# Optimization experiments

Measured on AMD Instinct MI355X. Metric: run time of the kernel, lower is better.

Reference implementation:

```python
import jax, jax.numpy as jnp
import numpy as np

EPS = 1e-6


def setup_inputs() -> dict:
    key = jax.random.key(0)
    k_x, k_qkv, k_proj = jax.random.split(key, 3)
    B, C, H, W, D = 4, 256, 16, 16, 16
    x = jax.random.normal(k_x, (B, C, H, W, D), dtype=jnp.float32)
    # 1x1 Conv3d == per-position linear; init roughly like torch conv default
    fan_in = C
    bound = 1.0 / np.sqrt(fan_in)
    qkv_w = jax.random.uniform(k_qkv, (3 * C, C), jnp.float32, -bound, bound)
    qkv_b = jnp.zeros((3 * C,), jnp.float32)
    proj_w = jax.random.uniform(k_proj, (C, C), jnp.float32, -bound, bound)
    proj_b = jnp.zeros((C,), jnp.float32)
    norm_gamma = jnp.ones((C,), jnp.float32)
    norm_beta = jnp.zeros((C,), jnp.float32)
    return {"x": x, "norm_gamma": norm_gamma, "norm_beta": norm_beta,
            "qkv_w": qkv_w, "qkv_b": qkv_b, "proj_w": proj_w, "proj_b": proj_b}


def reference(x, norm_gamma, norm_beta, qkv_w, qkv_b, proj_w, proj_b):
    B, C, H, W, D = x.shape
    N = H * W * D
    scale = float(C) ** -0.5

    # GroupNorm with num_groups=1: normalize over (C,H,W,D) per sample (biased var)
    mean = jnp.mean(x, axis=(1, 2, 3, 4), keepdims=True)
    var = jnp.mean(jnp.square(x - mean), axis=(1, 2, 3, 4), keepdims=True)
    xn = (x - mean) * jax.lax.rsqrt(var + EPS)
    xn = xn * norm_gamma[None, :, None, None, None] + norm_beta[None, :, None, None, None]

    xn_flat = xn.reshape(B, C, N)  # b c n
    # 1x1 conv == channel-mixing GEMM
    qkv = jnp.einsum('oc,bcn->bon', qkv_w, xn_flat) + qkv_b[None, :, None]  # [B, 3C, N]
    q, k, v = jnp.split(qkv, 3, axis=1)  # each [B, C, N]

    w = jnp.einsum('bcq,bck->bqk', q, k) * scale  # [B, N, N]
    w = jax.nn.softmax(w, axis=-1)
    h = jnp.einsum('bqk,bck->bcq', w, v)  # [B, C, N]

    h = jnp.einsum('oc,bcn->bon', proj_w, h) + proj_b[None, :, None]
    return x + h.reshape(B, C, H, W, D)
```

## Files before the change

### kernel.cpp

```cpp
#include <hip/hip_runtime.h>

typedef __attribute__((ext_vector_type(8))) short short8;
typedef __attribute__((ext_vector_type(4))) float f32x4;
typedef __attribute__((ext_vector_type(16))) float f32x16;
typedef __attribute__((ext_vector_type(4))) int i32x4;

__device__ __forceinline__ unsigned short f2bf(float f){
  union { float f; unsigned int u; } cv; cv.f = f;
  unsigned int u = cv.u;
  u = (u + 0x7fffu + ((u >> 16) & 1u)) >> 16;
  return (unsigned short)u;
}
__device__ __forceinline__ float bf2f(unsigned short h){
  union { unsigned int u; float f; } cv; cv.u = ((unsigned int)h) << 16;
  return cv.f;
}

typedef unsigned int u32g __attribute__((address_space(1)));
typedef unsigned int u32l __attribute__((address_space(3)));
__device__ __forceinline__ void gload16(const void* g, void* l){
  __builtin_amdgcn_global_load_lds((const u32g*)g, (u32l*)l, 16, 0, 0);
}

__device__ __forceinline__ unsigned int cvt2_fp8(float a, float b){
  unsigned int r;
  asm("v_cvt_pk_fp8_f32 %0, %1, %2" : "=v"(r) : "v"(a), "v"(b));
  return r;
}

#define BARRIER() asm volatile("s_barrier" ::: "memory")
#define WAITV(N)  asm volatile("s_waitcnt vmcnt(" #N ")" ::: "memory")

__global__ __launch_bounds__(256) void fused_pre_k(const float* __restrict__ x,
                                                   float2* __restrict__ partial,
                                                   const float* __restrict__ qkv_w,
                                                   const float* __restrict__ qkv_b,
                                                   const float* __restrict__ proj_w,
                                                   unsigned short* __restrict__ Wqk,
                                                   unsigned short* __restrict__ Wv,
                                                   unsigned short* __restrict__ Wp,
                                                   float* __restrict__ bias_qkv){
  const int blk = blockIdx.x;
  if (blk < 256){
    const int b = blk >> 6, xb = blk & 63;
    const float4* xp = (const float4*)(x + (size_t)b*1048576 + (size_t)xb*16384);
    float s = 0.f, sq = 0.f;
    #pragma unroll
    for (int i = 0; i < 16; ++i){
      float4 v = xp[threadIdx.x + i*256];
      s  += v.x + v.y + v.z + v.w;
      sq += v.x*v.x + v.y*v.y + v.z*v.z + v.w*v.w;
    }
    #pragma unroll
    for (int m = 1; m < 64; m <<= 1){ s += __shfl_xor(s, m); sq += __shfl_xor(sq, m); }
    __shared__ float2 acc[4];
    if ((threadIdx.x & 63) == 0) acc[threadIdx.x >> 6] = make_float2(s, sq);
    __syncthreads();
    if (threadIdx.x == 0){
      float S = 0.f, Q = 0.f;
      for (int i = 0; i < 4; ++i){ S += acc[i].x; Q += acc[i].y; }
      partial[b*64 + xb] = make_float2(S, Q);
    }
  } else {
    int id = (blk - 256) * 256 + threadIdx.x;
    if (id < 131072){
      Wqk[id] = f2bf(qkv_w[id]);
      if (id < 768) bias_qkv[id] = qkv_b[id];
    } else if (id < 196608){
      Wv[id - 131072] = f2bf(qkv_w[id]);
    } else {
      int j = id - 196608;
      Wp[j] = f2bf(proj_w[j]);
    }
  }
}

__global__ __launch_bounds__(256) void norm_transpose_k(const float* __restrict__ x,
                                                        const float* __restrict__ gamma,
                                                        const float* __restrict__ beta,
                                                        const float2* __restrict__ partial,
                                                        unsigned short* __restrict__ xnt){
  __shared__ float tile[64][65];
  __shared__ float2 stt;
  const int b = blockIdx.z, n0 = blockIdx.x*64, c0 = blockIdx.y*64;
  const int t = threadIdx.x;
  if (t < 64){
    float2 p = partial[b*64 + t];
    float s = p.x, q = p.y;
    #pragma unroll
    for (int m = 1; m < 64; m <<= 1){ s += __shfl_xor(s, m); q += __shfl_xor(q, m); }
    if (t == 0){
      const float inv = 1.0f/1048576.0f;
      float mean = s*inv;
      float var  = q*inv - mean*mean;
      stt = make_float2(mean, rsqrtf(var + 1e-6f));
    }
  }
  __syncthreads();
  const float2 st = stt;
  const int col = t & 63, rb = t >> 6;
  #pragma unroll
  for (int i = 0; i < 16; ++i){
    int rr = i*4 + rb;
    float xv = x[((size_t)b*256 + c0 + rr)*4096 + n0 + col];
    tile[rr][col] = (xv - st.x) * st.y * gamma[c0+rr] + beta[c0+rr];
  }
  __syncthreads();
  #pragma unroll
  for (int i = 0; i < 16; ++i){
    int nr = i*4 + rb;
    xnt[((size_t)b*4096 + n0 + nr)*256 + c0 + col] = f2bf(tile[col][nr]);
  }
}

__global__ __launch_bounds__(256) void gemm_nt_k(const unsigned short* __restrict__ A,
                                                 const unsigned short* __restrict__ B,
                                                 int lda, int ldb, long sA, long sB,
                                                 const float* __restrict__ bias_m,
                                                 const float* __restrict__ bias_n,
                                                 const float* __restrict__ resid, long sR,
                                                 float* __restrict__ outF,
                                                 unsigned short* __restrict__ outB,
                                                 unsigned char* __restrict__ out8,
                                                 unsigned char* __restrict__ out8v,
                                                 int ldc, long sC, int vtile){
  __shared__ unsigned short As[64][40];
  __shared__ unsigned short Bs[64][40];
  const int b  = blockIdx.z;
  const int m0 = blockIdx.x * 64, n0 = blockIdx.y * 64;
  const unsigned short* Ab = A + (size_t)b * sA;
  const unsigned short* Bb = B + (size_t)b * sB;
  const int t = threadIdx.x;
  const int lane = t & 63, w = t >> 6;
  const int g = lane >> 4, r = lane & 15;
  const int wm = (w >> 1) * 32, wn = (w & 1) * 32;
  const int lrow = t >> 2, lcol = (t & 3) * 8;
  f32x4 acc00 = {0,0,0,0}, acc01 = {0,0,0,0}, acc10 = {0,0,0,0}, acc11 = {0,0,0,0};
  for (int ks = 0; ks < 8; ++ks){
    short8 av = *(const short8*)(Ab + (size_t)(m0 + lrow) * lda + ks*32 + lcol);
    short8 bv = *(const short8*)(Bb + (size_t)(n0 + lrow) * ldb + ks*32 + lcol);
    __syncthreads();
    *(short8*)&As[lrow][lcol] = av;
    *(short8*)&Bs[lrow][lcol] = bv;
    __syncthreads();
    short8 af0 = *(const short8*)&As[wm + r][g*8];
    short8 af1 = *(const short8*)&As[wm + 16 + r][g*8];
    short8 bf0 = *(const short8*)&Bs[wn + r][g*8];
    short8 bf1 = *(const short8*)&Bs[wn + 16 + r][g*8];
    acc00 = __builtin_amdgcn_mfma_f32_16x16x32_bf16(af0, bf0, acc00, 0, 0, 0);
    acc01 = __builtin_amdgcn_mfma_f32_16x16x32_bf16(af0, bf1, acc01, 0, 0, 0);
    acc10 = __builtin_amdgcn_mfma_f32_16x16x32_bf16(af1, bf0, acc10, 0, 0, 0);
    acc11 = __builtin_amdgcn_mfma_f32_16x16x32_bf16(af1, bf1, acc11, 0, 0, 0);
  }
  f32x4 accs[2][2] = {{acc00, acc01},{acc10, acc11}};
  #pragma unroll
  for (int mi = 0; mi < 2; ++mi)
    #pragma unroll
    for (int ni = 0; ni < 2; ++ni)
      #pragma unroll
      for (int j = 0; j < 4; ++j){
        int gm = m0 + wm + mi*16 + g*4 + j;
        int gn = n0 + wn + ni*16 + r;
        float vv = accs[mi][ni][j];
        if (bias_m) vv += bias_m[gm];
        if (bias_n) vv += bias_n[gn];
        if (resid)  vv += resid[(size_t)b*sR + (size_t)gm*ldc + gn];
        if (out8){
          unsigned char v8 = (unsigned char)(cvt2_fp8(vv, vv) & 0xff);
          if (vtile == 3 && gn >= 512){
            int c = gn - 512, n = gm;
            int inner = (((c & 31)*16 + (n & 15)) ^ (((c >> 3) & 1) << 3));
            out8v[(size_t)b*1048576 + (size_t)((n >> 4)*8 + (c >> 5))*512 + inner] = v8;
          } else {
            out8[(size_t)b*sC + (size_t)gm*ldc + gn] = v8;
          }
        } else if (outB){
          outB[(size_t)b*sC + (size_t)gm*ldc + gn] = f2bf(vv);
        } else {
          outF[(size_t)b*sC + (size_t)gm*ldc + gn] = vv;
        }
      }
}

__global__ __launch_bounds__(256, 2) void attn_k(const unsigned char* __restrict__ qk8,
                                                 const unsigned char* __restrict__ vt8,
                                                 unsigned short* __restrict__ po,
                                                 float* __restrict__ ml){
  __shared__ __align__(16) char smem[32768];
  const int id = blockIdx.x;
  const int combo = id & 15, qb = id >> 4;
  const int b = combo >> 2, ks = combo & 3;
  const int q0 = qb * 128;
  const int t = threadIdx.x, lane = t & 63, w = t >> 6;
  const int hi = lane >> 5, l31 = lane & 31;
  const unsigned char* qkb = qk8 + (size_t)b * 4096 * 512;
  const unsigned char* vtb = vt8 + (size_t)b * 1048576;
  const float SQL2 = 0.0625f * 1.44269504088896340736f;

  unsigned long long qf[16];
  {
    const unsigned char* qrow = qkb + (size_t)(q0 + w*32 + l31) * 512;
    #pragma unroll
    for (int s = 0; s < 16; ++s) qf[s] = *(const unsigned long long*)(qrow + s*16 + hi*8);
  }

  auto stageK = [&](int kt, char* buf){
    const int kbase = ks*1024 + kt*32;
    #pragma unroll
    for (int i2 = 0; i2 < 2; ++i2){
      int ci = (w*2 + i2)*64 + lane;
      int r = ci >> 4;
      const unsigned char* src = qkb + (size_t)(kbase + r)*512 + 256
                               + (((ci & 15) ^ (r & 15)) * 16);
      gload16(src, buf + (w*2 + i2)*1024);
    }
  };
  auto stageV = [&](int kt, char* buf){
    const int kbase = ks*1024 + kt*32;
    #pragma unroll
    for (int i = 0; i < 2; ++i){
      int tp = (w*2 + i)*2;
      int tile = tp + (lane >> 5);
      const unsigned char* src = vtb + (size_t)((kbase >> 4) + (tile >> 3))*4096
                               + (tile & 7)*512 + (lane & 31)*16;
      gload16(src, buf + 8192 + tp*512);
    }
  };
  stageK(0, smem);
  stageV(0, smem);

  f32x16 O[8];
  #pragma unroll
  for (int cb = 0; cb < 8; ++cb)
    #pragma unroll
    for (int jj = 0; jj < 16; ++jj) O[cb][jj] = 0.f;
  float lrun = 0.f;
  const int ksw = (l31 & 15) << 4;
  const int vsw = ((l31 >> 3) & 1) << 3;
  const int vbase = l31*16 + hi*8;

  for (int kt = 0; kt < 32; ++kt){
    char* cur = smem + (kt & 1)*16384;
    char* nxt = smem + ((kt + 1) & 1)*16384;

    WAITV(0);
    BARRIER();

    int ktn = (kt < 31) ? kt + 1 : 31;
    stageK(ktn, nxt);
    stageV(ktn, nxt);

    f32x16 Sa, Sb;
    #pragma unroll
    for (int jj = 0; jj < 16; ++jj){ Sa[jj] = 0.f; Sb[jj] = 0.f; }
    const char* kp = cur + l31*256;
    __builtin_amdgcn_s_setprio(1);
    #pragma unroll
    for (int s = 0; s < 8; ++s){
      unsigned long long k0 = *(const unsigned long long*)(kp + (((2*s  )*16 + hi*8) ^ ksw));
      unsigned long long k1 = *(const unsigned long long*)(kp + (((2*s+1)*16 + hi*8) ^ ksw));
      Sa = __builtin_amdgcn_mfma_f32_32x32x16_fp8_fp8((long long)k0, (long long)qf[2*s  ], Sa, 0, 0, 0);
      Sb = __builtin_amdgcn_mfma_f32_32x32x16_fp8_fp8((long long)k1, (long long)qf[2*s+1], Sb, 0, 0, 0);
    }
    __builtin_amdgcn_s_setprio(0);

    float p[16];
    #pragma unroll
    for (int jj = 0; jj < 16; ++jj)
      p[jj] = __builtin_amdgcn_exp2f((Sa[jj] + Sb[jj]) * SQL2);
    lrun += ((p[0]+p[1]) + (p[2]+p[3])) + ((p[4]+p[5]) + (p[6]+p[7]))
          + ((p[8]+p[9]) + (p[10]+p[11])) + ((p[12]+p[13]) + (p[14]+p[15]));
    unsigned A0 = (unsigned)__builtin_amdgcn_cvt_pk_fp8_f32(p[0],  p[1],  0, false);
    A0 = (unsigned)__builtin_amdgcn_cvt_pk_fp8_f32(p[2],  p[3],  (int)A0, true);
    unsigned B0 = (unsigned)__builtin_amdgcn_cvt_pk_fp8_f32(p[4],  p[5],  0, false);
    B0 = (unsigned)__builtin_amdgcn_cvt_pk_fp8_f32(p[6],  p[7],  (int)B0, true);
    unsigned A1 = (unsigned)__builtin_amdgcn_cvt_pk_fp8_f32(p[8],  p[9],  0, false);
    A1 = (unsigned)__builtin_amdgcn_cvt_pk_fp8_f32(p[10], p[11], (int)A1, true);
    unsigned B1 = (unsigned)__builtin_amdgcn_cvt_pk_fp8_f32(p[12], p[13], 0, false);
    B1 = (unsigned)__builtin_amdgcn_cvt_pk_fp8_f32(p[14], p[15], (int)B1, true);
    asm("v_permlane32_swap_b32 %0, %1" : "+v"(A0), "+v"(B0));
    asm("v_permlane32_swap_b32 %0, %1" : "+v"(A1), "+v"(B1));
    long long pb0 = (long long)(((unsigned long long)B0 << 32) | A0);
    long long pb1 = (long long)(((unsigned long long)B1 << 32) | A1);

    const char* Vt = cur + 8192;
    __builtin_amdgcn_s_setprio(1);
    #pragma unroll
    for (int cb = 0; cb < 8; ++cb){
      unsigned long long v0 = *(const unsigned long long*)(Vt + (0*8 + cb)*512 + (vbase ^ vsw));
      O[cb] = __builtin_amdgcn_mfma_f32_32x32x16_fp8_fp8((long long)v0, pb0, O[cb], 0, 0, 0);
      unsigned long long v1 = *(const unsigned long long*)(Vt + (1*8 + cb)*512 + (vbase ^ vsw));
      O[cb] = __builtin_amdgcn_mfma_f32_32x32x16_fp8_fp8((long long)v1, pb1, O[cb], 0, 0, 0);
    }
    __builtin_amdgcn_s_setprio(0);
  }
  WAITV(0);

  float lf = lrun + __shfl_xor(lrun, 32);
  const int qg = q0 + w*32 + l31;
  unsigned short* pob = po + (size_t)combo * 1048576;
  #pragma unroll
  for (int cb = 0; cb < 8; ++cb)
    #pragma unroll
    for (int jj = 0; jj < 16; ++jj){
      int c = cb*32 + (jj & 3) + 8*(jj >> 2) + 4*hi;
      pob[(size_t)c*4096 + qg] = f2bf(O[cb][jj]);
    }
  if (lane < 32)
    ml[(size_t)combo*4096 + qg] = lf;
}

__global__ __launch_bounds__(256) void attn_merge_k(const unsigned short* __restrict__ po,
                                                    const float* __restrict__ ml,
                                                    unsigned short* __restrict__ ho){
  __shared__ float Of[64][261];
  const int b = blockIdx.y, q0 = blockIdx.x * 64;
  const int t = threadIdx.x, ql = t & 63, ci = t >> 6;
  const int q = q0 + ql;
  float L = 0.f;
  #pragma unroll
  for (int ksv = 0; ksv < 4; ++ksv)
    L += ml[(size_t)(b*4 + ksv)*4096 + q];
  float inv = 1.0f / L;
  float acc[64];
  #pragma unroll
  for (int i = 0; i < 64; ++i) acc[i] = 0.f;
  #pragma unroll
  for (int ksv = 0; ksv < 4; ++ksv){
    const unsigned short* pb = po + (size_t)(b*4 + ksv)*1048576 + q;
    #pragma unroll
    for (int i = 0; i < 64; ++i)
      acc[i] += bf2f(pb[(size_t)(ci + 4*i)*4096]);
  }
  #pragma unroll
  for (int i = 0; i < 64; ++i) Of[ql][ci + 4*i] = acc[i] * inv;
  __syncthreads();
  const int qr = t >> 2, sub = t & 3;
  const float* rowp = Of[qr];
  unsigned short* dst = ho + ((size_t)(b*4096 + q0 + qr))*256;
  #pragma unroll
  for (int jj = 0; jj < 8; ++jj){
    int c = sub*8 + jj*32;
    float4 v0 = *(const float4*)(rowp + c);
    float4 v1 = *(const float4*)(rowp + c + 4);
    short8 o;
    o[0] = (short)f2bf(v0.x); o[1] = (short)f2bf(v0.y);
    o[2] = (short)f2bf(v0.z); o[3] = (short)f2bf(v0.w);
    o[4] = (short)f2bf(v1.x); o[5] = (short)f2bf(v1.y);
    o[6] = (short)f2bf(v1.z); o[7] = (short)f2bf(v1.w);
    *(short8*)(dst + c) = o;
  }
}

extern "C" void kernel_launch(void* const* d_in, const int* in_sizes, int n_in,
                              void* d_out, int out_size, void* d_ws, size_t ws_size,
                              hipStream_t stream){
  const float* x      = (const float*)d_in[0];
  const float* gamma  = (const float*)d_in[1];
  const float* beta   = (const float*)d_in[2];
  const float* qkv_w  = (const float*)d_in[3];
  const float* qkv_b  = (const float*)d_in[4];
  const float* proj_w = (const float*)d_in[5];
  const float* proj_b = (const float*)d_in[6];
  float* out = (float*)d_out;
  char* ws = (char*)d_ws;

  float2* partial        = (float2*)(ws + 0);
  float*  bias_qkv       = (float*)(ws + 4096);
  unsigned short* Wqk    = (unsigned short*)(ws + 8192);
  unsigned short* Wv     = (unsigned short*)(ws + 270336);
  unsigned short* Wp     = (unsigned short*)(ws + 401408);
  unsigned short* xnt    = (unsigned short*)(ws + 532480);
  unsigned char*  qk8    = (unsigned char*)(ws + 8921088);
  unsigned char*  vt8    = (unsigned char*)(ws + 17309696);
  unsigned short* po     = (unsigned short*)(ws + 25698304);
  float*          ml     = (float*)(ws + 59252736);
  unsigned short* ho     = xnt;

  fused_pre_k<<<1280, 256, 0, stream>>>(x, partial, qkv_w, qkv_b, proj_w,
                                        Wqk, Wv, Wp, bias_qkv);
  norm_transpose_k<<<dim3(64,4,4), 256, 0, stream>>>(x, gamma, beta, partial, xnt);
  gemm_nt_k<<<dim3(64,12,4), 256, 0, stream>>>(xnt, Wqk, 256, 256, 4096L*256, 0,
      nullptr, bias_qkv, nullptr, 0, nullptr, nullptr, qk8, vt8, 512, 4096L*512, 3);
  attn_k<<<dim3(512), 256, 0, stream>>>(qk8, vt8, po, ml);
  attn_merge_k<<<dim3(64,4), 256, 0, stream>>>(po, ml, ho);
  gemm_nt_k<<<dim3(4,64,4), 256, 0, stream>>>(Wp, ho, 256, 256, 0, 4096L*256,
      proj_b, nullptr, x, 1048576L, out, nullptr, nullptr, nullptr, 4096, 1048576L, 0);
}
```

Baseline: 124.5 us.

## Double-buffer gemm_nt tiles via direct global-to-LDS loads with XOR swizzle

Replaces the register-staged load/store into padded LDS arrays with global_load_lds direct transfers into a double-buffered shared region. The next K-slice is prefetched while the current one is consumed, and a single barrier per iteration replaces two. An XOR swizzle on the 16-byte column chunks avoids bank conflicts without padding. The cost is twice the LDS footprint and a reliance on WAITV/BARRIER macros being correct for the async loads.

```diff
diff --git a/kernel.cpp b/kernel.cpp
--- a/kernel.cpp
+++ b/kernel.cpp
@@ -124,8 +124,7 @@
                                                  unsigned char* __restrict__ out8,
                                                  unsigned char* __restrict__ out8v,
                                                  int ldc, long sC, int vtile){
-  __shared__ unsigned short As[64][40];
-  __shared__ unsigned short Bs[64][40];
+  __shared__ __align__(16) char gs[16384];
   const int b  = blockIdx.z;
   const int m0 = blockIdx.x * 64, n0 = blockIdx.y * 64;
   const unsigned short* Ab = A + (size_t)b * sA;
@@ -134,19 +133,37 @@
   const int lane = t & 63, w = t >> 6;
   const int g = lane >> 4, r = lane & 15;
   const int wm = (w >> 1) * 32, wn = (w & 1) * 32;
-  const int lrow = t >> 2, lcol = (t & 3) * 8;
+  const int srow = lane >> 2;
+  const int scol = ((lane & 3) ^ (srow & 3)) * 8;
+  auto stage = [&](int ks, int half){
+    char* buf = gs + half*8192;
+    if (w < 2){
+      #pragma unroll
+      for (int i = 0; i < 2; ++i){
+        int m = w*32 + i*16 + srow;
+        gload16(Ab + (size_t)(m0 + m)*lda + ks*32 + scol, buf + w*2048 + i*1024);
+      }
+    } else {
+      #pragma unroll
+      for (int i = 0; i < 2; ++i){
+        int n = (w-2)*32 + i*16 + srow;
+        gload16(Bb + (size_t)(n0 + n)*ldb + ks*32 + scol, buf + 4096 + (w-2)*2048 + i*1024);
+      }
+    }
+  };
+  stage(0, 0);
   f32x4 acc00 = {0,0,0,0}, acc01 = {0,0,0,0}, acc10 = {0,0,0,0}, acc11 = {0,0,0,0};
+  const int sa = (g ^ (r & 3)) << 4;
   for (int ks = 0; ks < 8; ++ks){
-    short8 av = *(const short8*)(Ab + (size_t)(m0 + lrow) * lda + ks*32 + lcol);
-    short8 bv = *(const short8*)(Bb + (size_t)(n0 + lrow) * ldb + ks*32 + lcol);
-    __syncthreads();
-    *(short8*)&As[lrow][lcol] = av;
-    *(short8*)&Bs[lrow][lcol] = bv;
-    __syncthreads();
-    short8 af0 = *(const short8*)&As[wm + r][g*8];
-    short8 af1 = *(const short8*)&As[wm + 16 + r][g*8];
-    short8 bf0 = *(const short8*)&Bs[wn + r][g*8];
-    short8 bf1 = *(const short8*)&Bs[wn + 16 + r][g*8];
+    WAITV(0);
+    BARRIER();
+    if (ks < 7) stage(ks + 1, (ks + 1) & 1);
+    const char* Abuf = gs + (ks & 1)*8192;
+    const char* Bbuf = Abuf + 4096;
+    short8 af0 = *(const short8*)(Abuf + (wm + r)*64 + sa);
+    short8 af1 = *(const short8*)(Abuf + (wm + 16 + r)*64 + sa);
+    short8 bf0 = *(const short8*)(Bbuf + (wn + r)*64 + sa);
+    short8 bf1 = *(const short8*)(Bbuf + (wn + 16 + r)*64 + sa);
     acc00 = __builtin_amdgcn_mfma_f32_16x16x32_bf16(af0, bf0, acc00, 0, 0, 0);
     acc01 = __builtin_amdgcn_mfma_f32_16x16x32_bf16(af0, bf1, acc01, 0, 0, 0);
     acc10 = __builtin_amdgcn_mfma_f32_16x16x32_bf16(af1, bf0, acc10, 0, 0, 0);
```

Result: no change. 126.1 us (+1.3%).

## Fuse split-K attention merge into output projection GEMM with packed bf16 partials

Applied to the files above, without the earlier changes.

Replaces the separate attention-merge kernel and the projection GEMM with one kernel that sums the four split-K partial outputs on the fly, feeds them as MFMA operands against double-buffered Wp tiles, and applies 1/L normalisation, bias and residual in the epilogue. The attention kernel now writes its partial outputs as packed 4×bf16 64-bit stores in a channel-group-major layout, using the hardware pack-convert instruction, instead of scalar 16-bit stores. The QKV GEMM is specialised to its single fp8 output path, dropping runtime branches. This removes one launch and the round trip of the merged bf16 tensor through memory. In exchange the merge work is tied to GEMM tiling, and the fused kernel re-reads partials with only 32 columns per block.

```diff
diff --git a/kernel.cpp b/kernel.cpp
--- a/kernel.cpp
+++ b/kernel.cpp
@@ -22,6 +22,11 @@
   __builtin_amdgcn_global_load_lds((const u32g*)g, (u32l*)l, 16, 0, 0);
 }
 
+__device__ __forceinline__ unsigned int cvtpk_bf16(float lo, float hi){
+  unsigned int r;
+  asm("v_cvt_pk_bf16_f32 %0, %1, %2" : "=v"(r) : "v"(lo), "v"(hi));
+  return r;
+}
 __device__ __forceinline__ unsigned int cvt2_fp8(float a, float b){
   unsigned int r;
   asm("v_cvt_pk_fp8_f32 %0, %1, %2" : "=v"(r) : "v"(a), "v"(b));
@@ -116,14 +121,10 @@
 __global__ __launch_bounds__(256) void gemm_nt_k(const unsigned short* __restrict__ A,
                                                  const unsigned short* __restrict__ B,
                                                  int lda, int ldb, long sA, long sB,
-                                                 const float* __restrict__ bias_m,
                                                  const float* __restrict__ bias_n,
-                                                 const float* __restrict__ resid, long sR,
-                                                 float* __restrict__ outF,
-                                                 unsigned short* __restrict__ outB,
                                                  unsigned char* __restrict__ out8,
                                                  unsigned char* __restrict__ out8v,
-                                                 int ldc, long sC, int vtile){
+                                                 int ldc, long sC){
   __shared__ unsigned short As[64][40];
   __shared__ unsigned short Bs[64][40];
   const int b  = blockIdx.z;
@@ -161,30 +162,21 @@
       for (int j = 0; j < 4; ++j){
         int gm = m0 + wm + mi*16 + g*4 + j;
         int gn = n0 + wn + ni*16 + r;
-        float vv = accs[mi][ni][j];
-        if (bias_m) vv += bias_m[gm];
-        if (bias_n) vv += bias_n[gn];
-        if (resid)  vv += resid[(size_t)b*sR + (size_t)gm*ldc + gn];
-        if (out8){
-          unsigned char v8 = (unsigned char)(cvt2_fp8(vv, vv) & 0xff);
-          if (vtile == 3 && gn >= 512){
-            int c = gn - 512, n = gm;
-            int inner = (((c & 31)*16 + (n & 15)) ^ (((c >> 3) & 1) << 3));
-            out8v[(size_t)b*1048576 + (size_t)((n >> 4)*8 + (c >> 5))*512 + inner] = v8;
-          } else {
-            out8[(size_t)b*sC + (size_t)gm*ldc + gn] = v8;
-          }
-        } else if (outB){
-          outB[(size_t)b*sC + (size_t)gm*ldc + gn] = f2bf(vv);
+        float vv = accs[mi][ni][j] + bias_n[gn];
+        unsigned char v8 = (unsigned char)(cvt2_fp8(vv, vv) & 0xff);
+        if (gn >= 512){
+          int c = gn - 512, n = gm;
+          int inner = (((c & 31)*16 + (n & 15)) ^ (((c >> 3) & 1) << 3));
+          out8v[(size_t)b*1048576 + (size_t)((n >> 4)*8 + (c >> 5))*512 + inner] = v8;
         } else {
-          outF[(size_t)b*sC + (size_t)gm*ldc + gn] = vv;
+          out8[(size_t)b*sC + (size_t)gm*ldc + gn] = v8;
         }
       }
 }
 
 __global__ __launch_bounds__(256, 2) void attn_k(const unsigned char* __restrict__ qk8,
                                                  const unsigned char* __restrict__ vt8,
-                                                 unsigned short* __restrict__ po,
+                                                 char* __restrict__ po4,
                                                  float* __restrict__ ml){
   __shared__ __align__(16) char smem[32768];
   const int id = blockIdx.x;
@@ -298,57 +290,102 @@
 
   float lf = lrun + __shfl_xor(lrun, 32);
   const int qg = q0 + w*32 + l31;
-  unsigned short* pob = po + (size_t)combo * 1048576;
+  unsigned long long* pob = (unsigned long long*)(po4 + (size_t)combo * 2097152);
   #pragma unroll
   for (int cb = 0; cb < 8; ++cb)
     #pragma unroll
-    for (int jj = 0; jj < 16; ++jj){
-      int c = cb*32 + (jj & 3) + 8*(jj >> 2) + 4*hi;
-      pob[(size_t)c*4096 + qg] = f2bf(O[cb][jj]);
+    for (int J = 0; J < 4; ++J){
+      unsigned lo = cvtpk_bf16(O[cb][4*J+0], O[cb][4*J+1]);
+      unsigned hi2 = cvtpk_bf16(O[cb][4*J+2], O[cb][4*J+3]);
+      int cg = cb*8 + J*2 + hi;
+      pob[(size_t)cg*4096 + qg] = ((unsigned long long)hi2 << 32) | lo;
     }
   if (lane < 32)
     ml[(size_t)combo*4096 + qg] = lf;
 }
 
-__global__ __launch_bounds__(256) void attn_merge_k(const unsigned short* __restrict__ po,
-                                                    const float* __restrict__ ml,
-                                                    unsigned short* __restrict__ ho){
-  __shared__ float Of[64][261];
-  const int b = blockIdx.y, q0 = blockIdx.x * 64;
-  const int t = threadIdx.x, ql = t & 63, ci = t >> 6;
-  const int q = q0 + ql;
+__global__ __launch_bounds__(256, 2) void projm_k(const char* __restrict__ po4,
+                                                  const float* __restrict__ ml,
+                                                  const unsigned short* __restrict__ Wp,
+                                                  const float* __restrict__ proj_b,
+                                                  const float* __restrict__ x,
+                                                  float* __restrict__ out){
+  __shared__ __align__(16) char wsm[32768];
+  const int b = blockIdx.y, n0 = blockIdx.x * 32;
+  const int t = threadIdx.x, lane = t & 63, w = t >> 6;
+  const int hi = lane >> 5, l31 = lane & 31;
+  const int n = n0 + l31;
+
   float L = 0.f;
   #pragma unroll
-  for (int ksv = 0; ksv < 4; ++ksv)
-    L += ml[(size_t)(b*4 + ksv)*4096 + q];
+  for (int ksv = 0; ksv < 4; ++ksv) L += ml[(size_t)(b*4 + ksv)*4096 + n];
   float inv = 1.0f / L;
-  float acc[64];
-  #pragma unroll
-  for (int i = 0; i < 64; ++i) acc[i] = 0.f;
-  #pragma unroll
-  for (int ksv = 0; ksv < 4; ++ksv){
-    const unsigned short* pb = po + (size_t)(b*4 + ksv)*1048576 + q;
-    #pragma unroll
-    for (int i = 0; i < 64; ++i)
-      acc[i] += bf2f(pb[(size_t)(ci + 4*i)*4096]);
-  }
-  #pragma unroll
-  for (int i = 0; i < 64; ++i) Of[ql][ci + 4*i] = acc[i] * inv;
-  __syncthreads();
-  const int qr = t >> 2, sub = t & 3;
-  const float* rowp = Of[qr];
-  unsigned short* dst = ho + ((size_t)(b*4096 + q0 + qr))*256;
-  #pragma unroll
-  for (int jj = 0; jj < 8; ++jj){
-    int c = sub*8 + jj*32;
-    float4 v0 = *(const float4*)(rowp + c);
-    float4 v1 = *(const float4*)(rowp + c + 4);
-    short8 o;
-    o[0] = (short)f2bf(v0.x); o[1] = (short)f2bf(v0.y);
-    o[2] = (short)f2bf(v0.z); o[3] = (short)f2bf(v0.w);
-    o[4] = (short)f2bf(v1.x); o[5] = (short)f2bf(v1.y);
-    o[6] = (short)f2bf(v1.z); o[7] = (short)f2bf(v1.w);
-    *(short8*)(dst + c) = o;
+
+  const char* pob[4];
+  #pragma unroll
+  for (int ksv = 0; ksv < 4; ++ksv) pob[ksv] = po4 + (size_t)(b*4 + ksv)*2097152;
+
+  auto stageW = [&](int kstep, char* buf){
+    #pragma unroll
+    for (int i = 0; i < 4; ++i){
+      int tile = w*4 + i, ot = tile >> 1, ks2 = tile & 1;
+      const unsigned short* src = Wp + (size_t)(ot*32 + l31)*256 + kstep*32 + ks2*16 + hi*8;
+      gload16(src, buf + tile*1024);
+    }
+  };
+  stageW(0, wsm);
+
+  f32x16 acc0, acc1;
+  #pragma unroll
+  for (int jj = 0; jj < 16; ++jj){ acc0[jj] = 0.f; acc1[jj] = 0.f; }
+
+  for (int kstep = 0; kstep < 8; ++kstep){
+    char* cur = wsm + (kstep & 1)*16384;
+    char* nxt = wsm + ((kstep + 1) & 1)*16384;
+    WAITV(0);
+    BARRIER();
+    if (kstep < 7) stageW(kstep + 1, nxt);
+
+    short8 hf[2];
+    #pragma unroll
+    for (int ks2 = 0; ks2 < 2; ++ks2){
+      int cg = kstep*8 + ks2*4 + hi*2;
+      float s[8];
+      #pragma unroll
+      for (int j = 0; j < 8; ++j) s[j] = 0.f;
+      #pragma unroll
+      for (int ksv = 0; ksv < 4; ++ksv){
+        unsigned long long a = *(const unsigned long long*)(pob[ksv] + ((size_t)cg*4096 + n)*8);
+        unsigned long long c = *(const unsigned long long*)(pob[ksv] + ((size_t)(cg+1)*4096 + n)*8);
+        s[0] += bf2f((unsigned short)a);        s[1] += bf2f((unsigned short)(a >> 16));
+        s[2] += bf2f((unsigned short)(a >> 32));s[3] += bf2f((unsigned short)(a >> 48));
+        s[4] += bf2f((unsigned short)c);        s[5] += bf2f((unsigned short)(c >> 16));
+        s[6] += bf2f((unsigned short)(c >> 32));s[7] += bf2f((unsigned short)(c >> 48));
+      }
+      unsigned u0 = cvtpk_bf16(s[0], s[1]), u1 = cvtpk_bf16(s[2], s[3]);
+      unsigned u2 = cvtpk_bf16(s[4], s[5]), u3 = cvtpk_bf16(s[6], s[7]);
+      i32x4 uv = {(int)u0, (int)u1, (int)u2, (int)u3};
+      hf[ks2] = __builtin_bit_cast(short8, uv);
+    }
+
+    #pragma unroll
+    for (int ks2 = 0; ks2 < 2; ++ks2){
+      short8 wf0 = *(const short8*)(cur + ((w*2 + 0)*2 + ks2)*1024 + lane*16);
+      acc0 = __builtin_amdgcn_mfma_f32_32x32x16_bf16(wf0, hf[ks2], acc0, 0, 0, 0);
+      short8 wf1 = *(const short8*)(cur + ((w*2 + 1)*2 + ks2)*1024 + lane*16);
+      acc1 = __builtin_amdgcn_mfma_f32_32x32x16_bf16(wf1, hf[ks2], acc1, 0, 0, 0);
+    }
+  }
+
+  #pragma unroll
+  for (int ot = 0; ot < 2; ++ot){
+    const f32x16& A = ot ? acc1 : acc0;
+    #pragma unroll
+    for (int jj = 0; jj < 16; ++jj){
+      int o = w*64 + ot*32 + (jj & 3) + 8*(jj >> 2) + 4*hi;
+      size_t off = ((size_t)(b*256 + o))*4096 + n;
+      out[off] = A[jj]*inv + proj_b[o] + x[off];
+    }
   }
 }
 
@@ -373,17 +410,14 @@
   unsigned short* xnt    = (unsigned short*)(ws + 532480);
   unsigned char*  qk8    = (unsigned char*)(ws + 8921088);
   unsigned char*  vt8    = (unsigned char*)(ws + 17309696);
-  unsigned short* po     = (unsigned short*)(ws + 25698304);
+  char*           po4    = (char*)(ws + 25698304);
   float*          ml     = (float*)(ws + 59252736);
-  unsigned short* ho     = xnt;
 
   fused_pre_k<<<1280, 256, 0, stream>>>(x, partial, qkv_w, qkv_b, proj_w,
                                         Wqk, Wv, Wp, bias_qkv);
   norm_transpose_k<<<dim3(64,4,4), 256, 0, stream>>>(x, gamma, beta, partial, xnt);
   gemm_nt_k<<<dim3(64,12,4), 256, 0, stream>>>(xnt, Wqk, 256, 256, 4096L*256, 0,
-      nullptr, bias_qkv, nullptr, 0, nullptr, nullptr, qk8, vt8, 512, 4096L*512, 3);
-  attn_k<<<dim3(512), 256, 0, stream>>>(qk8, vt8, po, ml);
-  attn_merge_k<<<dim3(64,4), 256, 0, stream>>>(po, ml, ho);
-  gemm_nt_k<<<dim3(4,64,4), 256, 0, stream>>>(Wp, ho, 256, 256, 0, 4096L*256,
-      proj_b, nullptr, x, 1048576L, out, nullptr, nullptr, nullptr, 4096, 1048576L, 0);
-}
+      bias_qkv, qk8, vt8, 512, 4096L*512);
+  attn_k<<<dim3(512), 256, 0, stream>>>(qk8, vt8, po4, ml);
+  projm_k<<<dim3(128, 4), 256, 0, stream>>>(po4, ml, Wp, proj_b, x, out);
+}
```

Result: faster. 113.1 us (median of 3 runs) (-9.1%).
